# Performance work log

Measured on AMD Instinct MI355X. Metric: run time of the kernel, lower is better.

The kernel has to match this reference:

```python
import jax, jax.numpy as jnp
import numpy as np

N, IN_DIM, OUT_DIM = 8192, 1024, 256
AVG_DEG = 32


def _w(key, shape, scale=0.05):
    return jax.random.normal(key, shape, dtype=jnp.float32) * scale


def setup_inputs() -> dict:
    key = jax.random.key(0)
    ks = jax.random.split(key, 20)
    x = jax.random.normal(ks[0], (N, IN_DIM), dtype=jnp.float32)
    # binary adjacency with average degree ~AVG_DEG (adj_matrix_to_edge_index
    # only keeps indices, so edge weights are effectively 1)
    A_pos = (jax.random.uniform(ks[1], (N, N)) < (AVG_DEG / N)).astype(jnp.float32)
    d = {"x": x, "A_pos": A_pos}
    # Linear layers (stored as [in, out]; y = x @ W + b)
    d["W1"], d["b1"] = _w(ks[2], (IN_DIM, 256)), jnp.zeros((256,), jnp.float32)
    d["W2"], d["b2"] = _w(ks[3], (256, 62)), jnp.zeros((62,), jnp.float32)
    d["W3"], d["b3"] = _w(ks[4], (62, OUT_DIM)), jnp.zeros((OUT_DIM,), jnp.float32)
    # GCNConv weights/biases
    d["G1"], d["gb1"] = _w(ks[5], (256, 256)), jnp.zeros((256,), jnp.float32)
    d["G2"], d["gb2"] = _w(ks[6], (62, 62)), jnp.zeros((62,), jnp.float32)
    for i, k in zip(range(3, 7), ks[7:11]):
        d[f"G{i}"], d[f"gb{i}"] = _w(k, (OUT_DIM, OUT_DIM)), jnp.zeros((OUT_DIM,), jnp.float32)
    return d


def _gcn_forward(x, A_pos, W1, b1, W2, b2, W3, b3,
                 G1, gb1, G2, gb2, G3, gb3, G4, gb4, G5, gb5, G6, gb6):
    n = x.shape[0]
    # GCN symmetric normalization with self loops: D^{-1/2}(A+I)D^{-1/2}
    A_hat = A_pos + jnp.eye(n, dtype=x.dtype)
    deg = A_hat.sum(axis=1)
    dinv = jnp.where(deg > 0, deg ** -0.5, 0.0)
    A_norm = dinv[:, None] * A_hat * dinv[None, :]

    def gcn(h, W, b):
        return A_norm @ (h @ W) + b

    x1_lin = x @ W1 + b1
    x1 = x1_lin + jax.nn.relu(gcn(x1_lin, G1, gb1))
    x2_lin = x1 @ W2 + b2
    x2 = x2_lin + jax.nn.relu(gcn(x2_lin, G2, gb2))
    x3_lin = x2 @ W3 + b3
    w = 0.5  # self.weight before *= 0.5
    x3 = x3_lin + w * jax.nn.relu(gcn(x3_lin, G3, gb3))
    x4 = x3 + w * jax.nn.relu(gcn(x4_in := x3, G4, gb4))
    w = w * 0.5  # self.weight *= 0.5
    x5 = x4 + w * jax.nn.relu(gcn(x4, G5, gb5))
    x6 = x5 + w * gcn(x5, G6, gb6)
    return x6


def reference(x, A_pos, W1, b1, W2, b2, W3, b3,
              G1, gb1, G2, gb2, G3, gb3, G4, gb4, G5, gb5, G6, gb6):
    return _gcn_forward(x, A_pos, W1, b1, W2, b2, W3, b3,
                        G1, gb1, G2, gb2, G3, gb3, G4, gb4, G5, gb5, G6, gb6)
```

## Files before the change

kernel.cpp:

```cpp
#include <hip/hip_runtime.h>
#include <hip/hip_bf16.h>
#include <stddef.h>
#include <stdint.h>

#define NROWS 8192
#define MAXD 128

typedef __attribute__((ext_vector_type(8))) short bf16x8;
typedef __attribute__((ext_vector_type(4))) float f32x4;
typedef __attribute__((ext_vector_type(4))) unsigned short u16x4;

static __device__ __forceinline__ unsigned short f2bf(float f) {
    unsigned int u = __float_as_uint(f);
    unsigned int r = (u + 0x7FFFu + ((u >> 16) & 1u)) >> 16;
    return (unsigned short)r;
}
static __device__ __forceinline__ float bf2f(unsigned short h) {
    return __uint_as_float(((unsigned int)h) << 16);
}
static __device__ __forceinline__ f32x4 unpack4(uint2 u) {
    f32x4 f;
    f[0] = __uint_as_float(u.x << 16);
    f[1] = __uint_as_float(u.x & 0xFFFF0000u);
    f[2] = __uint_as_float(u.y << 16);
    f[3] = __uint_as_float(u.y & 0xFFFF0000u);
    return f;
}

__global__ __launch_bounds__(256) void build_adj(
    const float* __restrict__ A, int* __restrict__ ell,
    int* __restrict__ cnt, float* __restrict__ dinv)
{
    int row = blockIdx.x;
    const float4* arow = (const float4*)(A + (size_t)row * NROWS);
    __shared__ int scnt;
    if (threadIdx.x == 0) scnt = 0;
    __syncthreads();
    int* erow = ell + (size_t)row * MAXD;
    for (int q = threadIdx.x; q < NROWS / 4; q += 256) {
        float4 v = arow[q];
        int j = q * 4;
        if (v.x != 0.f) { int s = atomicAdd(&scnt, 1); if (s < MAXD) erow[s] = j; }
        if (v.y != 0.f) { int s = atomicAdd(&scnt, 1); if (s < MAXD) erow[s] = j + 1; }
        if (v.z != 0.f) { int s = atomicAdd(&scnt, 1); if (s < MAXD) erow[s] = j + 2; }
        if (v.w != 0.f) { int s = atomicAdd(&scnt, 1); if (s < MAXD) erow[s] = j + 3; }
    }
    __syncthreads();
    if (threadIdx.x == 0) {
        int c = scnt; if (c > MAXD) c = MAXD;
        cnt[row] = c;
        dinv[row] = rsqrtf((float)scnt + 1.0f);
    }
}

__global__ __launch_bounds__(256) void tconv(
    const float* __restrict__ W, unsigned short* __restrict__ ht,
    unsigned short* __restrict__ lt, int K, int N, int Kpad, int Npad)
{
    int idx = blockIdx.x * 256 + threadIdx.x;
    if (idx >= Npad * Kpad) return;
    int n = idx / Kpad, k = idx % Kpad;
    float v = (k < K && n < N) ? W[(size_t)k * N + n] : 0.f;
    unsigned short hv = f2bf(v);
    ht[idx] = hv;
    lt[idx] = f2bf(v - bf2f(hv));
}

__global__ __launch_bounds__(256) void tconvG5(
    const float* __restrict__ g1, const float* __restrict__ g3,
    const float* __restrict__ g4, const float* __restrict__ g5,
    const float* __restrict__ g6,
    unsigned short* __restrict__ h1, unsigned short* __restrict__ l1,
    unsigned short* __restrict__ h3, unsigned short* __restrict__ l3,
    unsigned short* __restrict__ h4, unsigned short* __restrict__ l4,
    unsigned short* __restrict__ h5, unsigned short* __restrict__ l5,
    unsigned short* __restrict__ h6, unsigned short* __restrict__ l6)
{
    const float* s; unsigned short* h; unsigned short* l;
    switch (blockIdx.y) {
        case 0:  s = g1; h = h1; l = l1; break;
        case 1:  s = g3; h = h3; l = l3; break;
        case 2:  s = g4; h = h4; l = l4; break;
        case 3:  s = g5; h = h5; l = l5; break;
        default: s = g6; h = h6; l = l6; break;
    }
    int idx = blockIdx.x * 256 + threadIdx.x;
    int n = idx >> 8, k = idx & 255;
    float v = s[(size_t)k * 256 + n];
    unsigned short hv = f2bf(v);
    h[idx] = hv;
    l[idx] = f2bf(v - bf2f(hv));
}

__global__ void pad2(const float* __restrict__ b2, const float* __restrict__ gb2,
                     float* __restrict__ b2p, float* __restrict__ gb2p)
{
    int i = threadIdx.x;
    if (i < 64) b2p[i] = (i < 62) ? b2[i] : 0.f;
    else { int j = i - 64; gb2p[j] = (j < 62) ? gb2[j] : 0.f; }
}

__global__ __launch_bounds__(256) void gemm_mfma(
    const float* __restrict__ A,
    const unsigned short* __restrict__ Bth, const unsigned short* __restrict__ Btl,
    const float* __restrict__ bias,
    float* __restrict__ C, unsigned short* __restrict__ Cb, int K, int N)
{
    __shared__ __attribute__((aligned(16))) char smem[49152];
    const int tid = threadIdx.x;
    const int lane = tid & 63;
    const int w = tid >> 6;
    const int bm0 = blockIdx.x * 128;
    const int bn0 = blockIdx.y * 64;
    const int m_off = (w & 1) * 64;
    const int n_off = (w >> 1) * 32;

    f32x4 acc[4][2];
#pragma unroll
    for (int i = 0; i < 4; i++)
#pragma unroll
        for (int j = 0; j < 2; j++) acc[i][j] = (f32x4){0.f, 0.f, 0.f, 0.f};

    for (int k0 = 0; k0 < K; k0 += 64) {
#pragma unroll
        for (int i = 0; i < 8; ++i) {
            int q = tid + i * 256;
            int row = q >> 4;
            int kq = (q & 15) * 4;
            f32x4 v = *(const f32x4*)(A + (size_t)(bm0 + row) * K + k0 + kq);
            u16x4 hv, lv;
#pragma unroll
            for (int j = 0; j < 4; ++j) {
                unsigned short hh = f2bf(v[j]);
                hv[j] = hh;
                lv[j] = f2bf(v[j] - bf2f(hh));
            }
            int logb = kq * 2;
            int swz = (row << 7) + (logb ^ ((row & 7) << 4));
            *(u16x4*)(smem + swz) = hv;
            *(u16x4*)(smem + 16384 + swz) = lv;
        }
#pragma unroll
        for (int i = 0; i < 4; ++i) {
            int c = tid + i * 256;
            int half = c >> 9;
            int cc = c & 511;
            int row = cc >> 3;
            int logb = (cc & 7) * 16;
            const unsigned short* s =
                (half ? Btl : Bth) + (size_t)(bn0 + row) * K + k0 + (logb >> 1);
            bf16x8 v = *(const bf16x8*)s;
            int swz = (row << 7) + (logb ^ ((row & 7) << 4));
            *(bf16x8*)(smem + 32768 + (half << 13) + swz) = v;
        }
        __syncthreads();

#pragma unroll
        for (int kk = 0; kk < 64; kk += 32) {
            bf16x8 ah[4], al[4], bh[2], bl[2];
            int kb = (kk + ((lane >> 4) * 8)) * 2;
#pragma unroll
            for (int mi = 0; mi < 4; mi++) {
                int row = m_off + mi * 16 + (lane & 15);
                int off = (row << 7) + (kb ^ ((row & 7) << 4));
                ah[mi] = *(const bf16x8*)(smem + off);
                al[mi] = *(const bf16x8*)(smem + 16384 + off);
            }
#pragma unroll
            for (int ni = 0; ni < 2; ni++) {
                int row = n_off + ni * 16 + (lane & 15);
                int off = (row << 7) + (kb ^ ((row & 7) << 4));
                bh[ni] = *(const bf16x8*)(smem + 32768 + off);
                bl[ni] = *(const bf16x8*)(smem + 40960 + off);
            }
#pragma unroll
            for (int mi = 0; mi < 4; mi++)
#pragma unroll
                for (int ni = 0; ni < 2; ni++) {
                    acc[mi][ni] = __builtin_amdgcn_mfma_f32_16x16x32_bf16(ah[mi], bh[ni], acc[mi][ni], 0, 0, 0);
                    acc[mi][ni] = __builtin_amdgcn_mfma_f32_16x16x32_bf16(ah[mi], bl[ni], acc[mi][ni], 0, 0, 0);
                    acc[mi][ni] = __builtin_amdgcn_mfma_f32_16x16x32_bf16(al[mi], bh[ni], acc[mi][ni], 0, 0, 0);
                }
        }
        __syncthreads();
    }

#pragma unroll
    for (int mi = 0; mi < 4; mi++)
#pragma unroll
        for (int ni = 0; ni < 2; ni++) {
            int col = bn0 + n_off + ni * 16 + (lane & 15);
            float bv = bias ? bias[col] : 0.f;
            int rbase = bm0 + m_off + mi * 16 + ((lane >> 4) * 4);
#pragma unroll
            for (int r = 0; r < 4; r++) {
                float v = acc[mi][ni][r] + bv;
                size_t idx = (size_t)(rbase + r) * N + col;
                if (C)  C[idx]  = v;
                if (Cb) Cb[idx] = f2bf(v);
            }
        }
}

__global__ __launch_bounds__(64) void spmm_bf(
    const unsigned short* __restrict__ Tb, const int* __restrict__ ell,
    const int* __restrict__ cnt, const float* __restrict__ dinv,
    const float* __restrict__ base, const float* __restrict__ gb,
    float* __restrict__ out, float wscale, int do_relu)
{
    __shared__ int nb[MAXD];
    __shared__ float dv[MAXD];
    int row = blockIdx.x;
    int t = threadIdx.x;
    int c = cnt[row];
    for (int e = t; e < c; e += 64) {
        int j = ell[(size_t)row * MAXD + e];
        nb[e] = j;
        dv[e] = dinv[j];
    }
    __syncthreads();
    float di = dinv[row];
    f32x4 r = unpack4(*(const uint2*)(Tb + (size_t)row * 256 + t * 4)) * di;
    f32x4 s1 = {0.f,0.f,0.f,0.f}, s2 = {0.f,0.f,0.f,0.f}, s3 = {0.f,0.f,0.f,0.f};
    int e = 0;
    for (; e + 4 <= c; e += 4) {
        uint2 v0 = *(const uint2*)(Tb + (size_t)nb[e]     * 256 + t * 4);
        uint2 v1 = *(const uint2*)(Tb + (size_t)nb[e + 1] * 256 + t * 4);
        uint2 v2 = *(const uint2*)(Tb + (size_t)nb[e + 2] * 256 + t * 4);
        uint2 v3 = *(const uint2*)(Tb + (size_t)nb[e + 3] * 256 + t * 4);
        r  += dv[e]     * unpack4(v0);
        s1 += dv[e + 1] * unpack4(v1);
        s2 += dv[e + 2] * unpack4(v2);
        s3 += dv[e + 3] * unpack4(v3);
    }
    for (; e < c; ++e)
        r += dv[e] * unpack4(*(const uint2*)(Tb + (size_t)nb[e] * 256 + t * 4));
    r = (r + s1) + (s2 + s3);
    f32x4 g = *(const f32x4*)(gb + t * 4);
    f32x4 b4 = *(const f32x4*)(base + (size_t)row * 256 + t * 4);
    f32x4 o4;
#pragma unroll
    for (int j = 0; j < 4; ++j) {
        float v = fmaf(di, r[j], g[j]);
        if (do_relu) v = fmaxf(v, 0.f);
        o4[j] = fmaf(wscale, v, b4[j]);
    }
    *(f32x4*)(out + (size_t)row * 256 + t * 4) = o4;
}

__global__ __launch_bounds__(64) void spmm64_bf(
    const unsigned short* __restrict__ Tb, const int* __restrict__ ell,
    const int* __restrict__ cnt, const float* __restrict__ dinv,
    const float* __restrict__ base, const float* __restrict__ gb,
    float* __restrict__ out)
{
    __shared__ int nb[MAXD];
    __shared__ float dv[MAXD];
    int row = blockIdx.x;
    int f = threadIdx.x;
    int c = cnt[row];
    for (int e = f; e < c; e += 64) {
        int j = ell[(size_t)row * MAXD + e];
        nb[e] = j;
        dv[e] = dinv[j];
    }
    __syncthreads();
    float di = dinv[row];
    float r = di * bf2f(Tb[(size_t)row * 64 + f]);
    float p1 = 0.f, p2 = 0.f, p3 = 0.f;
    int e = 0;
    for (; e + 4 <= c; e += 4) {
        r  = fmaf(dv[e],     bf2f(Tb[(size_t)nb[e]     * 64 + f]), r);
        p1 = fmaf(dv[e + 1], bf2f(Tb[(size_t)nb[e + 1] * 64 + f]), p1);
        p2 = fmaf(dv[e + 2], bf2f(Tb[(size_t)nb[e + 2] * 64 + f]), p2);
        p3 = fmaf(dv[e + 3], bf2f(Tb[(size_t)nb[e + 3] * 64 + f]), p3);
    }
    for (; e < c; ++e) r = fmaf(dv[e], bf2f(Tb[(size_t)nb[e] * 64 + f]), r);
    r = (r + p1) + (p2 + p3);
    float v = fmaf(di, r, gb[f]);
    v = fmaxf(v, 0.f);
    out[(size_t)row * 64 + f] = v + base[(size_t)row * 64 + f];
}

static inline void mfma(const float* A, const unsigned short* Bth,
                        const unsigned short* Btl, const float* bias,
                        float* C, unsigned short* Cb, int K, int N, hipStream_t s)
{
    dim3 grid(NROWS / 128, N / 64);
    gemm_mfma<<<grid, 256, 0, s>>>(A, Bth, Btl, bias, C, Cb, K, N);
}

extern "C" void kernel_launch(void* const* d_in, const int* in_sizes, int n_in,
                              void* d_out, int out_size, void* d_ws, size_t ws_size,
                              hipStream_t stream)
{
    const float* x    = (const float*)d_in[0];
    const float* Apos = (const float*)d_in[1];
    const float* W1 = (const float*)d_in[2];  const float* b1  = (const float*)d_in[3];
    const float* W2 = (const float*)d_in[4];  const float* b2  = (const float*)d_in[5];
    const float* W3 = (const float*)d_in[6];  const float* b3  = (const float*)d_in[7];
    const float* G1 = (const float*)d_in[8];  const float* gb1 = (const float*)d_in[9];
    const float* G2 = (const float*)d_in[10]; const float* gb2 = (const float*)d_in[11];
    const float* G3 = (const float*)d_in[12]; const float* gb3 = (const float*)d_in[13];
    const float* G4 = (const float*)d_in[14]; const float* gb4 = (const float*)d_in[15];
    const float* G5 = (const float*)d_in[16]; const float* gb5 = (const float*)d_in[17];
    const float* G6 = (const float*)d_in[18]; const float* gb6 = (const float*)d_in[19];

    char* ws = (char*)d_ws;
    size_t off = 0;
    auto alloc = [&](size_t bytes) -> void* {
        void* p = ws + off;
        off = (off + bytes + 255) & ~(size_t)255;
        return p;
    };
    int*   ell  = (int*)  alloc((size_t)NROWS * MAXD * 4);
    int*   cnt  = (int*)  alloc((size_t)NROWS * 4);
    float* dinv = (float*)alloc((size_t)NROWS * 4);
    unsigned short* W1th = (unsigned short*)alloc(256 * 1024 * 2);
    unsigned short* W1tl = (unsigned short*)alloc(256 * 1024 * 2);
    unsigned short* W2th = (unsigned short*)alloc(64 * 256 * 2);
    unsigned short* W2tl = (unsigned short*)alloc(64 * 256 * 2);
    unsigned short* W3th = (unsigned short*)alloc(256 * 64 * 2);
    unsigned short* W3tl = (unsigned short*)alloc(256 * 64 * 2);
    unsigned short* G1th = (unsigned short*)alloc(256 * 256 * 2);
    unsigned short* G1tl = (unsigned short*)alloc(256 * 256 * 2);
    unsigned short* G2th = (unsigned short*)alloc(64 * 64 * 2);
    unsigned short* G2tl = (unsigned short*)alloc(64 * 64 * 2);
    unsigned short* G3th = (unsigned short*)alloc(256 * 256 * 2);
    unsigned short* G3tl = (unsigned short*)alloc(256 * 256 * 2);
    unsigned short* G4th = (unsigned short*)alloc(256 * 256 * 2);
    unsigned short* G4tl = (unsigned short*)alloc(256 * 256 * 2);
    unsigned short* G5th = (unsigned short*)alloc(256 * 256 * 2);
    unsigned short* G5tl = (unsigned short*)alloc(256 * 256 * 2);
    unsigned short* G6th = (unsigned short*)alloc(256 * 256 * 2);
    unsigned short* G6tl = (unsigned short*)alloc(256 * 256 * 2);
    float* b2p  = (float*)alloc(64 * 4);
    float* gb2p = (float*)alloc(64 * 4);
    float* lin  = (float*)alloc((size_t)NROWS * 256 * 4);
    unsigned short* Tb = (unsigned short*)alloc((size_t)NROWS * 256 * 2);
    float* hA   = (float*)alloc((size_t)NROWS * 256 * 4);
    float* hB   = (float*)alloc((size_t)NROWS * 256 * 4);
    float* x2lin = lin;
    unsigned short* T62b = Tb;
    float* x2    = hB;
    float* outp = (float*)d_out;

    build_adj<<<NROWS, 256, 0, stream>>>(Apos, ell, cnt, dinv);

    tconv<<<(256 * 1024 + 255) / 256, 256, 0, stream>>>(W1, W1th, W1tl, 1024, 256, 1024, 256);
    tconv<<<(64 * 256 + 255) / 256, 256, 0, stream>>>(W2, W2th, W2tl, 256, 62, 256, 64);
    tconv<<<(256 * 64 + 255) / 256, 256, 0, stream>>>(W3, W3th, W3tl, 62, 256, 64, 256);
    tconv<<<(64 * 64 + 255) / 256, 256, 0, stream>>>(G2, G2th, G2tl, 62, 62, 64, 64);
    dim3 g5(256, 5);
    tconvG5<<<g5, 256, 0, stream>>>(G1, G3, G4, G5, G6,
                                    G1th, G1tl, G3th, G3tl, G4th, G4tl,
                                    G5th, G5tl, G6th, G6tl);
    pad2<<<1, 128, 0, stream>>>(b2, gb2, b2p, gb2p);

    mfma(x, W1th, W1tl, b1, lin, nullptr, 1024, 256, stream);
    mfma(lin, G1th, G1tl, nullptr, nullptr, Tb, 256, 256, stream);
    spmm_bf<<<NROWS, 64, 0, stream>>>(Tb, ell, cnt, dinv, lin, gb1, hA, 1.0f, 1);
    mfma(hA, W2th, W2tl, b2p, x2lin, nullptr, 256, 64, stream);
    mfma(x2lin, G2th, G2tl, nullptr, nullptr, T62b, 64, 64, stream);
    spmm64_bf<<<NROWS, 64, 0, stream>>>(T62b, ell, cnt, dinv, x2lin, gb2p, x2);
    mfma(x2, W3th, W3tl, b3, lin, nullptr, 64, 256, stream);
    mfma(lin, G3th, G3tl, nullptr, nullptr, Tb, 256, 256, stream);
    spmm_bf<<<NROWS, 64, 0, stream>>>(Tb, ell, cnt, dinv, lin, gb3, hB, 0.5f, 1);
    mfma(hB, G4th, G4tl, nullptr, nullptr, Tb, 256, 256, stream);
    spmm_bf<<<NROWS, 64, 0, stream>>>(Tb, ell, cnt, dinv, hB, gb4, hA, 0.5f, 1);
    mfma(hA, G5th, G5tl, nullptr, nullptr, Tb, 256, 256, stream);
    spmm_bf<<<NROWS, 64, 0, stream>>>(Tb, ell, cnt, dinv, hA, gb5, hB, 0.25f, 1);
    mfma(hB, G6th, G6tl, nullptr, nullptr, Tb, 256, 256, stream);
    spmm_bf<<<NROWS, 64, 0, stream>>>(Tb, ell, cnt, dinv, hB, gb6, outp, 0.25f, 0);
}
```

Baseline: 747.3 us.

## Fold linear and GCN weight products into concatenated GEMMs and merge prep kernels

Result: faster. 706.4 us (-5.5%).

```diff
diff --git a/kernel.cpp b/kernel.cpp
--- a/kernel.cpp
+++ b/kernel.cpp
@@ -27,84 +27,164 @@
     return f;
 }
 
-__global__ __launch_bounds__(256) void build_adj(
-    const float* __restrict__ A, int* __restrict__ ell,
-    int* __restrict__ cnt, float* __restrict__ dinv)
-{
-    int row = blockIdx.x;
-    const float4* arow = (const float4*)(A + (size_t)row * NROWS);
+__global__ __launch_bounds__(256) void prep_all(
+    const float* __restrict__ A,
+    int* __restrict__ ell, int* __restrict__ cnt, float* __restrict__ dinv,
+    const float* __restrict__ W1, const float* __restrict__ W2,
+    const float* __restrict__ W3,
+    const float* __restrict__ G1, const float* __restrict__ G2,
+    const float* __restrict__ G3, const float* __restrict__ G4,
+    const float* __restrict__ G5, const float* __restrict__ G6,
+    const float* __restrict__ b1, const float* __restrict__ b2,
+    const float* __restrict__ b3, const float* __restrict__ gb2,
+    unsigned short* __restrict__ B1h, unsigned short* __restrict__ B1l,
+    unsigned short* __restrict__ B2h, unsigned short* __restrict__ B2l,
+    unsigned short* __restrict__ B3h, unsigned short* __restrict__ B3l,
+    unsigned short* __restrict__ G4h, unsigned short* __restrict__ G4l,
+    unsigned short* __restrict__ G5h, unsigned short* __restrict__ G5l,
+    unsigned short* __restrict__ G6h, unsigned short* __restrict__ G6l,
+    float* __restrict__ bc1, float* __restrict__ bc2,
+    float* __restrict__ bc3, float* __restrict__ gb2p)
+{
     __shared__ int scnt;
-    if (threadIdx.x == 0) scnt = 0;
-    __syncthreads();
-    int* erow = ell + (size_t)row * MAXD;
-    for (int q = threadIdx.x; q < NROWS / 4; q += 256) {
-        float4 v = arow[q];
-        int j = q * 4;
-        if (v.x != 0.f) { int s = atomicAdd(&scnt, 1); if (s < MAXD) erow[s] = j; }
-        if (v.y != 0.f) { int s = atomicAdd(&scnt, 1); if (s < MAXD) erow[s] = j + 1; }
-        if (v.z != 0.f) { int s = atomicAdd(&scnt, 1); if (s < MAXD) erow[s] = j + 2; }
-        if (v.w != 0.f) { int s = atomicAdd(&scnt, 1); if (s < MAXD) erow[s] = j + 3; }
-    }
-    __syncthreads();
-    if (threadIdx.x == 0) {
-        int c = scnt; if (c > MAXD) c = MAXD;
-        cnt[row] = c;
-        dinv[row] = rsqrtf((float)scnt + 1.0f);
-    }
-}
-
-__global__ __launch_bounds__(256) void tconv(
-    const float* __restrict__ W, unsigned short* __restrict__ ht,
-    unsigned short* __restrict__ lt, int K, int N, int Kpad, int Npad)
-{
-    int idx = blockIdx.x * 256 + threadIdx.x;
-    if (idx >= Npad * Kpad) return;
-    int n = idx / Kpad, k = idx % Kpad;
-    float v = (k < K && n < N) ? W[(size_t)k * N + n] : 0.f;
-    unsigned short hv = f2bf(v);
-    ht[idx] = hv;
-    lt[idx] = f2bf(v - bf2f(hv));
-}
-
-__global__ __launch_bounds__(256) void tconvG5(
-    const float* __restrict__ g1, const float* __restrict__ g3,
-    const float* __restrict__ g4, const float* __restrict__ g5,
-    const float* __restrict__ g6,
-    unsigned short* __restrict__ h1, unsigned short* __restrict__ l1,
-    unsigned short* __restrict__ h3, unsigned short* __restrict__ l3,
-    unsigned short* __restrict__ h4, unsigned short* __restrict__ l4,
-    unsigned short* __restrict__ h5, unsigned short* __restrict__ l5,
-    unsigned short* __restrict__ h6, unsigned short* __restrict__ l6)
-{
-    const float* s; unsigned short* h; unsigned short* l;
-    switch (blockIdx.y) {
-        case 0:  s = g1; h = h1; l = l1; break;
-        case 1:  s = g3; h = h3; l = l3; break;
-        case 2:  s = g4; h = h4; l = l4; break;
-        case 3:  s = g5; h = h5; l = l5; break;
-        default: s = g6; h = h6; l = l6; break;
-    }
-    int idx = blockIdx.x * 256 + threadIdx.x;
-    int n = idx >> 8, k = idx & 255;
-    float v = s[(size_t)k * 256 + n];
-    unsigned short hv = f2bf(v);
-    h[idx] = hv;
-    l[idx] = f2bf(v - bf2f(hv));
-}
-
-__global__ void pad2(const float* __restrict__ b2, const float* __restrict__ gb2,
-                     float* __restrict__ b2p, float* __restrict__ gb2p)
-{
-    int i = threadIdx.x;
-    if (i < 64) b2p[i] = (i < 62) ? b2[i] : 0.f;
-    else { int j = i - 64; gb2p[j] = (j < 62) ? gb2[j] : 0.f; }
+    int b = blockIdx.x;
+    int tid = threadIdx.x;
+
+    if (b < 8192) {
+        int row = b;
+        const float4* arow = (const float4*)(A + (size_t)row * NROWS);
+        if (tid == 0) scnt = 0;
+        __syncthreads();
+        int* erow = ell + (size_t)row * MAXD;
+        for (int q = tid; q < NROWS / 4; q += 256) {
+            float4 v = arow[q];
+            int j = q * 4;
+            if (v.x != 0.f) { int s = atomicAdd(&scnt, 1); if (s < MAXD) erow[s] = j; }
+            if (v.y != 0.f) { int s = atomicAdd(&scnt, 1); if (s < MAXD) erow[s] = j + 1; }
+            if (v.z != 0.f) { int s = atomicAdd(&scnt, 1); if (s < MAXD) erow[s] = j + 2; }
+            if (v.w != 0.f) { int s = atomicAdd(&scnt, 1); if (s < MAXD) erow[s] = j + 3; }
+        }
+        __syncthreads();
+        if (tid == 0) {
+            int c = scnt; if (c > MAXD) c = MAXD;
+            cnt[row] = c;
+            dinv[row] = rsqrtf((float)scnt + 1.0f);
+        }
+        return;
+    }
+    b -= 8192;
+    if (b < 1024) {
+        int k = b, n = tid;
+        float v = W1[(size_t)k * 256 + n];
+        unsigned short h = f2bf(v);
+        B1h[(size_t)n * 1024 + k] = h;
+        B1l[(size_t)n * 1024 + k] = f2bf(v - bf2f(h));
+        return;
+    }
+    b -= 1024;
+    if (b < 1024) {
+        int k = b, n = tid;
+        float s = 0.f;
+        for (int j = 0; j < 256; ++j)
+            s = fmaf(W1[(size_t)k * 256 + j], G1[(size_t)j * 256 + n], s);
+        unsigned short h = f2bf(s);
+        B1h[(size_t)(256 + n) * 1024 + k] = h;
+        B1l[(size_t)(256 + n) * 1024 + k] = f2bf(s - bf2f(h));
+        return;
+    }
+    b -= 1024;
+    if (b < 256) {
+        if (tid < 64) {
+            int k = b, n = tid;
+            float v = (n < 62) ? W2[(size_t)k * 62 + n] : 0.f;
+            unsigned short h = f2bf(v);
+            B2h[(size_t)n * 256 + k] = h;
+            B2l[(size_t)n * 256 + k] = f2bf(v - bf2f(h));
+        }
+        return;
+    }
+    b -= 256;
+    if (b < 256) {
+        if (tid < 64) {
+            int k = b, n = tid;
+            float s = 0.f;
+            if (n < 62)
+                for (int j = 0; j < 62; ++j)
+                    s = fmaf(W2[(size_t)k * 62 + j], G2[(size_t)j * 62 + n], s);
+            unsigned short h = f2bf(s);
+            B2h[(size_t)(64 + n) * 256 + k] = h;
+            B2l[(size_t)(64 + n) * 256 + k] = f2bf(s - bf2f(h));
+        }
+        return;
+    }
+    b -= 256;
+    if (b < 64) {
+        int k = b, n = tid;
+        float v = (k < 62) ? W3[(size_t)k * 256 + n] : 0.f;
+        unsigned short h = f2bf(v);
+        B3h[(size_t)n * 64 + k] = h;
+        B3l[(size_t)n * 64 + k] = f2bf(v - bf2f(h));
+        return;
+    }
+    b -= 64;
+    if (b < 64) {
+        int k = b, n = tid;
+        float s = 0.f;
+        if (k < 62)
+            for (int j = 0; j < 256; ++j)
+                s = fmaf(W3[(size_t)k * 256 + j], G3[(size_t)j * 256 + n], s);
+        unsigned short h = f2bf(s);
+        B3h[(size_t)(256 + n) * 64 + k] = h;
+        B3l[(size_t)(256 + n) * 64 + k] = f2bf(s - bf2f(h));
+        return;
+    }
+    b -= 64;
+    if (b < 768) {
+        int g = b >> 8, k = b & 255, n = tid;
+        const float* src = (g == 0) ? G4 : (g == 1) ? G5 : G6;
+        unsigned short* hh = (g == 0) ? G4h : (g == 1) ? G5h : G6h;
+        unsigned short* ll = (g == 0) ? G4l : (g == 1) ? G5l : G6l;
+        float v = src[(size_t)k * 256 + n];
+        unsigned short h = f2bf(v);
+        hh[(size_t)n * 256 + k] = h;
+        ll[(size_t)n * 256 + k] = f2bf(v - bf2f(h));
+        return;
+    }
+    b -= 768;
+    if (b == 0) {
+        bc1[tid] = b1[tid];
+    } else if (b == 1) {
+        float s = 0.f;
+        for (int j = 0; j < 256; ++j) s = fmaf(b1[j], G1[(size_t)j * 256 + tid], s);
+        bc1[256 + tid] = s;
+    } else if (b == 2) {
+        if (tid < 64) {
+            bc2[tid] = (tid < 62) ? b2[tid] : 0.f;
+        } else if (tid < 128) {
+            int n = tid - 64;
+            float s = 0.f;
+            if (n < 62)
+                for (int j = 0; j < 62; ++j) s = fmaf(b2[j], G2[(size_t)j * 62 + n], s);
+            bc2[64 + n] = s;
+        } else if (tid < 192) {
+            int n = tid - 128;
+            gb2p[n] = (n < 62) ? gb2[n] : 0.f;
+        }
+    } else if (b == 3) {
+        bc3[tid] = b3[tid];
+    } else if (b == 4) {
+        float s = 0.f;
+        for (int j = 0; j < 256; ++j) s = fmaf(b3[j], G3[(size_t)j * 256 + tid], s);
+        bc3[256 + tid] = s;
+    }
 }
 
 __global__ __launch_bounds__(256) void gemm_mfma(
     const float* __restrict__ A,
     const unsigned short* __restrict__ Bth, const unsigned short* __restrict__ Btl,
     const float* __restrict__ bias,
-    float* __restrict__ C, unsigned short* __restrict__ Cb, int K, int N)
+    float* __restrict__ C, unsigned short* __restrict__ Cb,
+    int K, int N, int nsplit)
 {
     __shared__ __attribute__((aligned(16))) char smem[49152];
     const int tid = threadIdx.x;
@@ -185,6 +265,7 @@
         __syncthreads();
     }
 
+    const int wb = N - nsplit;
 #pragma unroll
     for (int mi = 0; mi < 4; mi++)
 #pragma unroll
@@ -195,9 +276,10 @@
 #pragma unroll
             for (int r = 0; r < 4; r++) {
                 float v = acc[mi][ni][r] + bv;
-                size_t idx = (size_t)(rbase + r) * N + col;
-                if (C)  C[idx]  = v;
-                if (Cb) Cb[idx] = f2bf(v);
+                if (col < nsplit)
+                    C[(size_t)(rbase + r) * nsplit + col] = v;
+                else
+                    Cb[(size_t)(rbase + r) * wb + (col - nsplit)] = f2bf(v);
             }
         }
 }
@@ -284,10 +366,11 @@
 
 static inline void mfma(const float* A, const unsigned short* Bth,
                         const unsigned short* Btl, const float* bias,
-                        float* C, unsigned short* Cb, int K, int N, hipStream_t s)
+                        float* C, unsigned short* Cb, int K, int N, int nsplit,
+                        hipStream_t s)
 {
     dim3 grid(NROWS / 128, N / 64);
-    gemm_mfma<<<grid, 256, 0, s>>>(A, Bth, Btl, bias, C, Cb, K, N);
+    gemm_mfma<<<grid, 256, 0, s>>>(A, Bth, Btl, bias, C, Cb, K, N, nsplit);
 }
 
 extern "C" void kernel_launch(void* const* d_in, const int* in_sizes, int n_in,
@@ -316,25 +399,21 @@
     int*   ell  = (int*)  alloc((size_t)NROWS * MAXD * 4);
     int*   cnt  = (int*)  alloc((size_t)NROWS * 4);
     float* dinv = (float*)alloc((size_t)NROWS * 4);
-    unsigned short* W1th = (unsigned short*)alloc(256 * 1024 * 2);
-    unsigned short* W1tl = (unsigned short*)alloc(256 * 1024 * 2);
-    unsigned short* W2th = (unsigned short*)alloc(64 * 256 * 2);
-    unsigned short* W2tl = (unsigned short*)alloc(64 * 256 * 2);
-    unsigned short* W3th = (unsigned short*)alloc(256 * 64 * 2);
-    unsigned short* W3tl = (unsigned short*)alloc(256 * 64 * 2);
-    unsigned short* G1th = (unsigned short*)alloc(256 * 256 * 2);
-    unsigned short* G1tl = (unsigned short*)alloc(256 * 256 * 2);
-    unsigned short* G2th = (unsigned short*)alloc(64 * 64 * 2);
-    unsigned short* G2tl = (unsigned short*)alloc(64 * 64 * 2);
-    unsigned short* G3th = (unsigned short*)alloc(256 * 256 * 2);
-    unsigned short* G3tl = (unsigned short*)alloc(256 * 256 * 2);
-    unsigned short* G4th = (unsigned short*)alloc(256 * 256 * 2);
-    unsigned short* G4tl = (unsigned short*)alloc(256 * 256 * 2);
-    unsigned short* G5th = (unsigned short*)alloc(256 * 256 * 2);
-    unsigned short* G5tl = (unsigned short*)alloc(256 * 256 * 2);
-    unsigned short* G6th = (unsigned short*)alloc(256 * 256 * 2);
-    unsigned short* G6tl = (unsigned short*)alloc(256 * 256 * 2);
-    float* b2p  = (float*)alloc(64 * 4);
+    unsigned short* B1h = (unsigned short*)alloc(512 * 1024 * 2);
+    unsigned short* B1l = (unsigned short*)alloc(512 * 1024 * 2);
+    unsigned short* B2h = (unsigned short*)alloc(128 * 256 * 2);
+    unsigned short* B2l = (unsigned short*)alloc(128 * 256 * 2);
+    unsigned short* B3h = (unsigned short*)alloc(512 * 64 * 2);
+    unsigned short* B3l = (unsigned short*)alloc(512 * 64 * 2);
+    unsigned short* G4h = (unsigned short*)alloc(256 * 256 * 2);
+    unsigned short* G4l = (unsigned short*)alloc(256 * 256 * 2);
+    unsigned short* G5h = (unsigned short*)alloc(256 * 256 * 2);
+    unsigned short* G5l = (unsigned short*)alloc(256 * 256 * 2);
+    unsigned short* G6h = (unsigned short*)alloc(256 * 256 * 2);
+    unsigned short* G6l = (unsigned short*)alloc(256 * 256 * 2);
+    float* bc1  = (float*)alloc(512 * 4);
+    float* bc2  = (float*)alloc(128 * 4);
+    float* bc3  = (float*)alloc(512 * 4);
     float* gb2p = (float*)alloc(64 * 4);
     float* lin  = (float*)alloc((size_t)NROWS * 256 * 4);
     unsigned short* Tb = (unsigned short*)alloc((size_t)NROWS * 256 * 2);
@@ -345,31 +424,22 @@
     float* x2    = hB;
     float* outp = (float*)d_out;
 
-    build_adj<<<NROWS, 256, 0, stream>>>(Apos, ell, cnt, dinv);
-
-    tconv<<<(256 * 1024 + 255) / 256, 256, 0, stream>>>(W1, W1th, W1tl, 1024, 256, 1024, 256);
-    tconv<<<(64 * 256 + 255) / 256, 256, 0, stream>>>(W2, W2th, W2tl, 256, 62, 256, 64);
-    tconv<<<(256 * 64 + 255) / 256, 256, 0, stream>>>(W3, W3th, W3tl, 62, 256, 64, 256);
-    tconv<<<(64 * 64 + 255) / 256, 256, 0, stream>>>(G2, G2th, G2tl, 62, 62, 64, 64);
-    dim3 g5(256, 5);
-    tconvG5<<<g5, 256, 0, stream>>>(G1, G3, G4, G5, G6,
-                                    G1th, G1tl, G3th, G3tl, G4th, G4tl,
-                                    G5th, G5tl, G6th, G6tl);
-    pad2<<<1, 128, 0, stream>>>(b2, gb2, b2p, gb2p);
-
-    mfma(x, W1th, W1tl, b1, lin, nullptr, 1024, 256, stream);
-    mfma(lin, G1th, G1tl, nullptr, nullptr, Tb, 256, 256, stream);
+    prep_all<<<11653, 256, 0, stream>>>(
+        Apos, ell, cnt, dinv, W1, W2, W3, G1, G2, G3, G4, G5, G6,
+        b1, b2, b3, gb2,
+        B1h, B1l, B2h, B2l, B3h, B3l, G4h, G4l, G5h, G5l, G6h, G6l,
+        bc1, bc2, bc3, gb2p);
+
+    mfma(x, B1h, B1l, bc1, lin, Tb, 1024, 512, 256, stream);
     spmm_bf<<<NROWS, 64, 0, stream>>>(Tb, ell, cnt, dinv, lin, gb1, hA, 1.0f, 1);
-    mfma(hA, W2th, W2tl, b2p, x2lin, nullptr, 256, 64, stream);
-    mfma(x2lin, G2th, G2tl, nullptr, nullptr, T62b, 64, 64, stream);
+    mfma(hA, B2h, B2l, bc2, x2lin, T62b, 256, 128, 64, stream);
     spmm64_bf<<<NROWS, 64, 0, stream>>>(T62b, ell, cnt, dinv, x2lin, gb2p, x2);
-    mfma(x2, W3th, W3tl, b3, lin, nullptr, 64, 256, stream);
-    mfma(lin, G3th, G3tl, nullptr, nullptr, Tb, 256, 256, stream);
+    mfma(x2, B3h, B3l, bc3, lin, Tb, 64, 512, 256, stream);
     spmm_bf<<<NROWS, 64, 0, stream>>>(Tb, ell, cnt, dinv, lin, gb3, hB, 0.5f, 1);
-    mfma(hB, G4th, G4tl, nullptr, nullptr, Tb, 256, 256, stream);
+    mfma(hB, G4h, G4l, nullptr, nullptr, Tb, 256, 256, 0, stream);
     spmm_bf<<<NROWS, 64, 0, stream>>>(Tb, ell, cnt, dinv, hB, gb4, hA, 0.5f, 1);
-    mfma(hA, G5th, G5tl, nullptr, nullptr, Tb, 256, 256, stream);
+    mfma(hA, G5h, G5l, nullptr, nullptr, Tb, 256, 256, 0, stream);
     spmm_bf<<<NROWS, 64, 0, stream>>>(Tb, ell, cnt, dinv, hA, gb5, hB, 0.25f, 1);
-    mfma(hB, G6th, G6tl, nullptr, nullptr, Tb, 256, 256, stream);
+    mfma(hB, G6h, G6l, nullptr, nullptr, Tb, 256, 256, 0, stream);
     spmm_bf<<<NROWS, 64, 0, stream>>>(Tb, ell, cnt, dinv, hB, gb6, outp, 0.25f, 0);
 }
```
